# Kernel optimization log

Measured on AMD Instinct MI355X. Metric: run time of the kernel, lower is better.

Reference implementation:

```python
import jax, jax.numpy as jnp
import numpy as np

B, L, D, N, K = 4, 4096, 1024, 64, 3
EPS = 1e-6

def setup_inputs() -> dict:
    key = jax.random.key(0)
    ks = jax.random.split(key, 24)
    f32 = jnp.float32
    inp = {
        'T': jax.random.normal(ks[0], (B, L, D), f32),
        'norm_scale': jnp.ones((D,), f32),
        'in_w': jax.random.normal(ks[1], (2 * D, D), f32) * (1.0 / np.sqrt(D)),
        'in_b': jnp.zeros((2 * D,), f32),
        'dw_w': jax.random.normal(ks[2], (D, 1, K), f32) * (1.0 / np.sqrt(K)),
        'dw_b': jnp.zeros((D,), f32),
        'pw_w': jax.random.normal(ks[3], (D, D), f32) * (1.0 / np.sqrt(D)),
        'pw_b': jnp.zeros((D,), f32),
        'f_win': jax.random.normal(ks[4], (N, D), f32) * (1.0 / np.sqrt(D)),
        'f_wout': jax.random.normal(ks[5], (D, N), f32) * (1.0 / np.sqrt(N)),
        'f_logA': jax.random.normal(ks[6], (N,), f32) * 0.02,
        'f_B': jax.random.normal(ks[7], (N,), f32) * 0.02,
        'f_C': jax.random.normal(ks[8], (N,), f32) * 0.02,
        'f_logdt': jnp.array(0.0, f32),
        'b_win': jax.random.normal(ks[9], (N, D), f32) * (1.0 / np.sqrt(D)),
        'b_wout': jax.random.normal(ks[10], (D, N), f32) * (1.0 / np.sqrt(N)),
        'b_logA': jax.random.normal(ks[11], (N,), f32) * 0.02,
        'b_B': jax.random.normal(ks[12], (N,), f32) * 0.02,
        'b_C': jax.random.normal(ks[13], (N,), f32) * 0.02,
        'b_logdt': jnp.array(0.0, f32),
        'out_w': jax.random.normal(ks[14], (D, D), f32) * (1.0 / np.sqrt(D)),
        'out_b': jnp.zeros((D,), f32),
    }
    return inp

def _ssm(x, win, wout, logA, Bp, Cp, logdt):
    # ZOH discretization of diagonal SSM
    dt = jnp.exp(logdt)
    A = -jnp.exp(logA)
    Abar = jnp.exp(A * dt)
    denom = jnp.where(jnp.abs(A) < EPS, jnp.ones_like(A), A)
    frac = jnp.where(jnp.abs(A) < EPS, dt, (Abar - 1.0) / denom)
    Bbar = frac * Bp
    u = jnp.einsum('bld,nd->bln', x, win)  # (B,L,N)
    h0 = jnp.zeros((x.shape[0], win.shape[0]), x.dtype)
    def step(h, ut):
        h = h * Abar + ut * Bbar
        return h, h * Cp
    _, ys = jax.lax.scan(step, h0, jnp.swapaxes(u, 0, 1))  # (L,B,N)
    y = jnp.swapaxes(ys, 0, 1)
    return jnp.einsum('bln,dn->bld', y, wout)

def reference(T, norm_scale, in_w, in_b, dw_w, dw_b, pw_w, pw_b,
              f_win, f_wout, f_logA, f_B, f_C, f_logdt,
              b_win, b_wout, b_logA, b_B, b_C, b_logdt,
              out_w, out_b):
    # RMSNorm
    rms = jnp.sqrt(jnp.mean(T * T, axis=-1, keepdims=True) + EPS)
    Tn = T / rms * norm_scale
    # in_linear -> chunk
    xz = Tn @ in_w.T + in_b
    x, z = jnp.split(xz, 2, axis=-1)
    gate = jax.nn.sigmoid(z)
    # depthwise-separable conv1d (NCH layout)
    xc = jnp.swapaxes(x, 1, 2)  # (B,D,L)
    xc = jax.lax.conv_general_dilated(
        xc, dw_w, window_strides=(1,), padding=[(K // 2, K // 2)],
        dimension_numbers=('NCH', 'OIH', 'NCH'), feature_group_count=D)
    xc = xc + dw_b[None, :, None]
    xc = jnp.einsum('bdl,ed->bel', xc, pw_w) + pw_b[None, :, None]
    x_conv = jnp.swapaxes(xc, 1, 2)  # (B,L,D)
    # bidirectional SSM
    y_f = _ssm(x_conv, f_win, f_wout, f_logA, f_B, f_C, f_logdt)
    y_b = _ssm(jnp.flip(x_conv, axis=1), b_win, b_wout, b_logA, b_B, b_C, b_logdt)
    y_b = jnp.flip(y_b, axis=1)
    y = (y_f + y_b) * gate
    y = y @ out_w.T + out_b
    return T + y
```

## Files before the change

kernel.cpp:

```cpp
#include <hip/hip_runtime.h>
#include <cstdint>


#define L_SEQ 4096
#define D_DIM 1024
#define B_SZ 4
#define M_TOK (B_SZ * L_SEQ)
#define CHUNKS 64
#define CLEN (L_SEQ / CHUNKS)

typedef short bf16x8 __attribute__((ext_vector_type(8)));
typedef float floatx4 __attribute__((ext_vector_type(4)));

__device__ inline unsigned short f2bf(float f) {
  union { float f; unsigned int u; } v; v.f = f;
  unsigned int r = v.u + 0x7FFFu + ((v.u >> 16) & 1u);
  return (unsigned short)(r >> 16);
}
__device__ inline float bf2f(unsigned short h) {
  union { unsigned int u; float f; } v; v.u = ((unsigned int)h) << 16;
  return v.f;
}

__device__ inline void load_lds16(const unsigned short* g, unsigned short* l) {
  __builtin_amdgcn_global_load_lds(
      (const __attribute__((address_space(1))) unsigned int*)g,
      (__attribute__((address_space(3))) unsigned int*)l, 16, 0, 0);
}

__global__ __launch_bounds__(256) void rmsnorm_kernel(
    const float* __restrict__ T, const float* __restrict__ scale,
    unsigned short* __restrict__ Tn) {
  int tok = blockIdx.x;
  int t = threadIdx.x;
  const float4* row = (const float4*)(T + (size_t)tok * D_DIM);
  float4 v = row[t];
  float ss = v.x*v.x + v.y*v.y + v.z*v.z + v.w*v.w;
  #pragma unroll
  for (int off = 32; off > 0; off >>= 1) ss += __shfl_down(ss, off);
  __shared__ float part[4];
  if ((t & 63) == 0) part[t >> 6] = ss;
  __syncthreads();
  float total = part[0] + part[1] + part[2] + part[3];
  float rinv = rsqrtf(total * (1.0f / D_DIM) + 1e-6f);
  const float4* sc4 = (const float4*)scale;
  float4 s = sc4[t];
  ushort4 o;
  o.x = f2bf(v.x * rinv * s.x); o.y = f2bf(v.y * rinv * s.y);
  o.z = f2bf(v.z * rinv * s.z); o.w = f2bf(v.w * rinv * s.w);
  ((ushort4*)(Tn + (size_t)tok * D_DIM))[t] = o;
}

__global__ __launch_bounds__(256) void f2bf_vec_kernel(
    const float* __restrict__ in, unsigned short* __restrict__ out, int n4) {
  int i = blockIdx.x * 256 + threadIdx.x;
  if (i < n4) {
    float4 v = ((const float4*)in)[i];
    ushort4 o; o.x = f2bf(v.x); o.y = f2bf(v.y); o.z = f2bf(v.z); o.w = f2bf(v.w);
    ((ushort4*)out)[i] = o;
  }
}

__global__ void prepack_kernel(
    const float* __restrict__ f_win, const float* __restrict__ b_win,
    const float* __restrict__ f_wout, const float* __restrict__ b_wout,
    unsigned short* __restrict__ Wu, unsigned short* __restrict__ Wy) {
  int i = blockIdx.x * blockDim.x + threadIdx.x;
  if (i < 128 * D_DIM) {
    int n = i >> 10, k = i & (D_DIM - 1);
    Wu[i] = f2bf((n < 64) ? f_win[n * D_DIM + k] : b_win[(n - 64) * D_DIM + k]);
    int d = i >> 7, kk = i & 127;
    Wy[i] = f2bf((kk < 64) ? f_wout[d * 64 + kk] : b_wout[d * 64 + (kk - 64)]);
  }
}

template<int MODE, typename OUT_T>
__global__ __launch_bounds__(256) void gemm_mfma_kernel(
    const unsigned short* __restrict__ A, const unsigned short* __restrict__ Bw,
    const float* __restrict__ bias, OUT_T* __restrict__ out,
    int M, int N, int Kt,
    const void* __restrict__ aux0, unsigned short* __restrict__ aux1) {
  __shared__ unsigned short As[2 * 128 * 32];
  __shared__ unsigned short Bs[2 * 128 * 32];
  int tid = threadIdx.x;
  int wave = tid >> 6, lane = tid & 63;
  int quad = lane >> 4, lrow = lane & 15;
  int bm = blockIdx.y * 128, bn = blockIdx.x * 128;
  int wm = (wave & 1) * 64, wn = (wave >> 1) * 64;

  int r0 = tid >> 2;
  int c8 = (tid & 3) * 8;
  const unsigned short* Ag0 = A  + (size_t)(bm + r0) * Kt + c8;
  const unsigned short* Ag1 = A  + (size_t)(bm + 64 + r0) * Kt + c8;
  const unsigned short* Bg0 = Bw + (size_t)(bn + r0) * Kt + c8;
  const unsigned short* Bg1 = Bw + (size_t)(bn + 64 + r0) * Kt + c8;
  unsigned short* Al0 = As + (size_t)wave * 512;
  unsigned short* Al1 = As + 2048 + (size_t)wave * 512;
  unsigned short* Bl0 = Bs + (size_t)wave * 512;
  unsigned short* Bl1 = Bs + 2048 + (size_t)wave * 512;

  floatx4 acc[4][4] = {};
  for (int k0 = 0; k0 < Kt; k0 += 64) {
    load_lds16(Ag0 + k0, Al0);
    load_lds16(Ag1 + k0, Al1);
    load_lds16(Bg0 + k0, Bl0);
    load_lds16(Bg1 + k0, Bl1);
    load_lds16(Ag0 + k0 + 32, Al0 + 4096);
    load_lds16(Ag1 + k0 + 32, Al1 + 4096);
    load_lds16(Bg0 + k0 + 32, Bl0 + 4096);
    load_lds16(Bg1 + k0 + 32, Bl1 + 4096);
    __syncthreads();
    #pragma unroll
    for (int ks = 0; ks < 2; ++ks) {
      const unsigned short* Ab = As + ks * 4096;
      const unsigned short* Bb = Bs + ks * 4096;
      bf16x8 af[4], bfr[4];
      #pragma unroll
      for (int mi = 0; mi < 4; ++mi)
        af[mi] = *(const bf16x8*)(Ab + (wm + mi * 16 + lrow) * 32 + quad * 8);
      #pragma unroll
      for (int ni = 0; ni < 4; ++ni)
        bfr[ni] = *(const bf16x8*)(Bb + (wn + ni * 16 + lrow) * 32 + quad * 8);
      #pragma unroll
      for (int mi = 0; mi < 4; ++mi)
        #pragma unroll
        for (int ni = 0; ni < 4; ++ni)
          acc[mi][ni] = __builtin_amdgcn_mfma_f32_16x16x32_bf16(
              af[mi], bfr[ni], acc[mi][ni], 0, 0, 0);
    }
    __syncthreads();
  }

  #pragma unroll
  for (int mi = 0; mi < 4; ++mi) {
    #pragma unroll
    for (int ni = 0; ni < 4; ++ni) {
      #pragma unroll
      for (int r = 0; r < 4; ++r) {
        int m = bm + wm + mi * 16 + quad * 4 + r;
        int n = bn + wn + ni * 16 + lrow;
        float v = acc[mi][ni][r];
        if (MODE == 0) {
          if (bias) v += bias[n];
          if (sizeof(OUT_T) == 2) out[(size_t)m * N + n] = (OUT_T)f2bf(v);
          else                    out[(size_t)m * N + n] = (OUT_T)v;
        } else if (MODE == 1) {
          if (bias) v += bias[n];
          if (n < D_DIM) ((unsigned short*)out)[(size_t)m * D_DIM + n] = f2bf(v);
          else aux1[(size_t)m * D_DIM + (n - D_DIM)] = f2bf(1.0f / (1.0f + expf(-v)));
        } else if (MODE == 2) {
          v *= bf2f(((const unsigned short*)aux0)[(size_t)m * N + n]);
          ((unsigned short*)out)[(size_t)m * N + n] = f2bf(v);
        } else {
          if (bias) v += bias[n];
          v += ((const float*)aux0)[(size_t)m * N + n];
          ((float*)out)[(size_t)m * N + n] = v;
        }
      }
    }
  }
}

__global__ __launch_bounds__(256) void dwconv_kernel(
    const unsigned short* __restrict__ x, const float* __restrict__ w,
    const float* __restrict__ b, unsigned short* __restrict__ out) {
  size_t i8 = (size_t)blockIdx.x * 256 + threadIdx.x;
  int d8 = (int)(i8 & (D_DIM / 8 - 1));
  size_t tok = i8 >> 7;
  int l = (int)(tok & (L_SEQ - 1));
  int d0 = d8 * 8;
  size_t base = tok * D_DIM + d0;
  bf16x8 cur = *(const bf16x8*)(x + base);
  float acc[8];
  #pragma unroll
  for (int j = 0; j < 8; ++j) {
    int d = d0 + j;
    acc[j] = b[d] + w[d * 3 + 1] * bf2f((unsigned short)cur[j]);
  }
  if (l > 0) {
    bf16x8 prv = *(const bf16x8*)(x + base - D_DIM);
    #pragma unroll
    for (int j = 0; j < 8; ++j) acc[j] += w[(d0 + j) * 3 + 0] * bf2f((unsigned short)prv[j]);
  }
  if (l < L_SEQ - 1) {
    bf16x8 nxt = *(const bf16x8*)(x + base + D_DIM);
    #pragma unroll
    for (int j = 0; j < 8; ++j) acc[j] += w[(d0 + j) * 3 + 2] * bf2f((unsigned short)nxt[j]);
  }
  bf16x8 o;
  #pragma unroll
  for (int j = 0; j < 8; ++j) o[j] = (short)f2bf(acc[j]);
  *(bf16x8*)(out + base) = o;
}

__device__ inline void ssm_params(
    int col,
    const float* f_logA, const float* f_B, const float* f_C, const float* f_logdt,
    const float* b_logA, const float* b_B, const float* b_C, const float* b_logdt,
    float& Abar, float& Bbar, float& Cc, float& Aa, float& dt) {
  int dir = col >> 6, n = col & 63;
  const float* logA  = dir ? b_logA  : f_logA;
  const float* Bp    = dir ? b_B     : f_B;
  const float* Cp    = dir ? b_C     : f_C;
  const float* logdt = dir ? b_logdt : f_logdt;
  dt = expf(logdt[0]);
  Aa = -expf(logA[n]);
  Abar = expf(Aa * dt);
  float frac = (fabsf(Aa) < 1e-6f) ? dt : (Abar - 1.0f) / Aa;
  Bbar = frac * Bp[n];
  Cc = Cp[n];
}

__global__ __launch_bounds__(128) void scan_s1_kernel(
    const float* __restrict__ u, float* __restrict__ states,
    const float* __restrict__ f_logA, const float* __restrict__ f_B,
    const float* __restrict__ f_C, const float* __restrict__ f_logdt,
    const float* __restrict__ b_logA, const float* __restrict__ b_B,
    const float* __restrict__ b_C, const float* __restrict__ b_logdt) {
  int col = threadIdx.x;
  int chunk = blockIdx.x, b = blockIdx.y;
  float Abar, Bbar, Cc, Aa, dt;
  ssm_params(col, f_logA, f_B, f_C, f_logdt, b_logA, b_B, b_C, b_logdt,
             Abar, Bbar, Cc, Aa, dt);
  size_t base = ((size_t)b * L_SEQ + (size_t)chunk * CLEN) * 128 + col;
  float h = 0.0f;
  if (col < 64) {
    for (int i0 = 0; i0 < CLEN; i0 += 8) {
      float uv[8];
      #pragma unroll
      for (int j = 0; j < 8; ++j) uv[j] = u[base + (size_t)(i0 + j) * 128];
      #pragma unroll
      for (int j = 0; j < 8; ++j) h = h * Abar + uv[j] * Bbar;
    }
  } else {
    for (int i0 = CLEN - 1; i0 >= 0; i0 -= 8) {
      float uv[8];
      #pragma unroll
      for (int j = 0; j < 8; ++j) uv[j] = u[base + (size_t)(i0 - j) * 128];
      #pragma unroll
      for (int j = 0; j < 8; ++j) h = h * Abar + uv[j] * Bbar;
    }
  }
  states[((size_t)b * CHUNKS + chunk) * 128 + col] = h;
}

__global__ __launch_bounds__(512) void scan_s2_kernel(
    const float* __restrict__ states, float* __restrict__ carries,
    const float* __restrict__ f_logA, const float* __restrict__ f_B,
    const float* __restrict__ f_C, const float* __restrict__ f_logdt,
    const float* __restrict__ b_logA, const float* __restrict__ b_B,
    const float* __restrict__ b_C, const float* __restrict__ b_logdt) {
  int tid = threadIdx.x;
  int b = tid >> 7, col = tid & 127;
  float Abar, Bbar, Cc, Aa, dt;
  ssm_params(col, f_logA, f_B, f_C, f_logdt, b_logA, b_B, b_C, b_logdt,
             Abar, Bbar, Cc, Aa, dt);
  float Ac = expf(Aa * dt * (float)CLEN);
  size_t sb = (size_t)b * CHUNKS * 128 + col;
  float cur = 0.0f;
  if (col < 64) {
    for (int c = 0; c < CHUNKS; ++c) {
      carries[sb + (size_t)c * 128] = cur;
      cur = cur * Ac + states[sb + (size_t)c * 128];
    }
  } else {
    for (int c = CHUNKS - 1; c >= 0; --c) {
      carries[sb + (size_t)c * 128] = cur;
      cur = cur * Ac + states[sb + (size_t)c * 128];
    }
  }
}

__global__ __launch_bounds__(128) void scan_s3_kernel(
    const float* __restrict__ u, const float* __restrict__ carries,
    unsigned short* __restrict__ y,
    const float* __restrict__ f_logA, const float* __restrict__ f_B,
    const float* __restrict__ f_C, const float* __restrict__ f_logdt,
    const float* __restrict__ b_logA, const float* __restrict__ b_B,
    const float* __restrict__ b_C, const float* __restrict__ b_logdt) {
  int col = threadIdx.x;
  int chunk = blockIdx.x, b = blockIdx.y;
  float Abar, Bbar, Cc, Aa, dt;
  ssm_params(col, f_logA, f_B, f_C, f_logdt, b_logA, b_B, b_C, b_logdt,
             Abar, Bbar, Cc, Aa, dt);
  size_t base = ((size_t)b * L_SEQ + (size_t)chunk * CLEN) * 128 + col;
  float h = carries[((size_t)b * CHUNKS + chunk) * 128 + col];
  if (col < 64) {
    for (int i0 = 0; i0 < CLEN; i0 += 8) {
      float uv[8];
      #pragma unroll
      for (int j = 0; j < 8; ++j) uv[j] = u[base + (size_t)(i0 + j) * 128];
      #pragma unroll
      for (int j = 0; j < 8; ++j) {
        h = h * Abar + uv[j] * Bbar;
        y[base + (size_t)(i0 + j) * 128] = f2bf(h * Cc);
      }
    }
  } else {
    for (int i0 = CLEN - 1; i0 >= 0; i0 -= 8) {
      float uv[8];
      #pragma unroll
      for (int j = 0; j < 8; ++j) uv[j] = u[base + (size_t)(i0 - j) * 128];
      #pragma unroll
      for (int j = 0; j < 8; ++j) {
        h = h * Abar + uv[j] * Bbar;
        y[base + (size_t)(i0 - j) * 128] = f2bf(h * Cc);
      }
    }
  }
}

extern "C" void kernel_launch(void* const* d_in, const int* in_sizes, int n_in,
                              void* d_out, int out_size, void* d_ws, size_t ws_size,
                              hipStream_t stream) {
  const float* T         = (const float*)d_in[0];
  const float* norm_scale= (const float*)d_in[1];
  const float* in_w      = (const float*)d_in[2];
  const float* in_b      = (const float*)d_in[3];
  const float* dw_w      = (const float*)d_in[4];
  const float* dw_b      = (const float*)d_in[5];
  const float* pw_w      = (const float*)d_in[6];
  const float* pw_b      = (const float*)d_in[7];
  const float* f_win     = (const float*)d_in[8];
  const float* f_wout    = (const float*)d_in[9];
  const float* f_logA    = (const float*)d_in[10];
  const float* f_B       = (const float*)d_in[11];
  const float* f_C       = (const float*)d_in[12];
  const float* f_logdt   = (const float*)d_in[13];
  const float* b_win     = (const float*)d_in[14];
  const float* b_wout    = (const float*)d_in[15];
  const float* b_logA    = (const float*)d_in[16];
  const float* b_B       = (const float*)d_in[17];
  const float* b_C       = (const float*)d_in[18];
  const float* b_logdt   = (const float*)d_in[19];
  const float* out_w     = (const float*)d_in[20];
  const float* out_b     = (const float*)d_in[21];
  float* out = (float*)d_out;

  char* ws = (char*)d_ws;
  const size_t MD = (size_t)M_TOK * D_DIM;
  unsigned short* gate  = (unsigned short*)ws;              ws += MD * 2;
  unsigned short* bufA  = (unsigned short*)ws;              ws += MD * 2;
  unsigned short* bufB  = (unsigned short*)ws;              ws += MD * 2;
  float*          u     = (float*)ws;                       ws += (size_t)M_TOK * 128 * 4;
  unsigned short* ybuf  = (unsigned short*)ws;              ws += (size_t)M_TOK * 128 * 2;
  unsigned short* w_in  = (unsigned short*)ws;              ws += (size_t)2 * D_DIM * D_DIM * 2;
  unsigned short* w_pw  = (unsigned short*)ws;              ws += (size_t)D_DIM * D_DIM * 2;
  unsigned short* w_out = (unsigned short*)ws;              ws += (size_t)D_DIM * D_DIM * 2;
  unsigned short* Wu    = (unsigned short*)ws;              ws += (size_t)128 * D_DIM * 2;
  unsigned short* Wy    = (unsigned short*)ws;              ws += (size_t)128 * D_DIM * 2;
  float*          states= (float*)ws;                       ws += (size_t)B_SZ * CHUNKS * 128 * 4;
  float*          carries=(float*)ws;

  f2bf_vec_kernel<<<(2 * D_DIM * D_DIM / 4 + 255) / 256, 256, 0, stream>>>(in_w, w_in, 2 * D_DIM * D_DIM / 4);
  f2bf_vec_kernel<<<(D_DIM * D_DIM / 4 + 255) / 256, 256, 0, stream>>>(pw_w, w_pw, D_DIM * D_DIM / 4);
  f2bf_vec_kernel<<<(D_DIM * D_DIM / 4 + 255) / 256, 256, 0, stream>>>(out_w, w_out, D_DIM * D_DIM / 4);
  prepack_kernel<<<(128 * D_DIM) / 256, 256, 0, stream>>>(f_win, b_win, f_wout, b_wout, Wu, Wy);
  rmsnorm_kernel<<<M_TOK, 256, 0, stream>>>(T, norm_scale, bufA);
  {
    dim3 g((2 * D_DIM) / 128, M_TOK / 128);
    gemm_mfma_kernel<1, unsigned short><<<g, 256, 0, stream>>>(
        bufA, w_in, in_b, bufB, M_TOK, 2 * D_DIM, D_DIM, nullptr, gate);
  }
  dwconv_kernel<<<(MD / 8) / 256, 256, 0, stream>>>(bufB, dw_w, dw_b, bufA);
  {
    dim3 g(D_DIM / 128, M_TOK / 128);
    gemm_mfma_kernel<0, unsigned short><<<g, 256, 0, stream>>>(
        bufA, w_pw, pw_b, bufB, M_TOK, D_DIM, D_DIM, nullptr, nullptr);
  }
  {
    dim3 g(1, M_TOK / 128);
    gemm_mfma_kernel<0, float><<<g, 256, 0, stream>>>(
        bufB, Wu, nullptr, u, M_TOK, 128, D_DIM, nullptr, nullptr);
  }
  {
    dim3 g1(CHUNKS, B_SZ);
    scan_s1_kernel<<<g1, 128, 0, stream>>>(u, states, f_logA, f_B, f_C, f_logdt,
                                           b_logA, b_B, b_C, b_logdt);
    scan_s2_kernel<<<1, 512, 0, stream>>>(states, carries, f_logA, f_B, f_C, f_logdt,
                                          b_logA, b_B, b_C, b_logdt);
    scan_s3_kernel<<<g1, 128, 0, stream>>>(u, carries, ybuf, f_logA, f_B, f_C, f_logdt,
                                           b_logA, b_B, b_C, b_logdt);
  }
  {
    dim3 g(D_DIM / 128, M_TOK / 128);
    gemm_mfma_kernel<2, unsigned short><<<g, 256, 0, stream>>>(
        ybuf, Wy, nullptr, bufA, M_TOK, D_DIM, 128, gate, nullptr);
  }
  {
    dim3 g(D_DIM / 128, M_TOK / 128);
    gemm_mfma_kernel<3, float><<<g, 256, 0, stream>>>(
        bufA, w_out, out_b, out, M_TOK, D_DIM, D_DIM, T, nullptr);
  }
}
```

Baseline: 634.7 us.

## Double-buffer GEMM LDS tiles to overlap global loads with MFMA compute

The GEMM main loop now splits LDS into two buffers of a 32-wide K slice each. It prefetches the next slice into the other buffer while the MFMAs run on the current one, so each iteration needs one barrier instead of two. It also raises wave priority around the MFMA block with s_setprio. The loop runs twice as many iterations with half the work each, so per-iteration overhead grows. How much overlap is gained depends on how load_lds16 is implemented (direct-to-LDS versus through registers).

```diff
diff --git a/kernel.cpp b/kernel.cpp
--- a/kernel.cpp
+++ b/kernel.cpp
@@ -80,8 +80,8 @@
     const float* __restrict__ bias, OUT_T* __restrict__ out,
     int M, int N, int Kt,
     const void* __restrict__ aux0, unsigned short* __restrict__ aux1) {
-  __shared__ unsigned short As[2 * 128 * 32];
-  __shared__ unsigned short Bs[2 * 128 * 32];
+  __shared__ unsigned short As[2][128 * 32];
+  __shared__ unsigned short Bs[2][128 * 32];
   int tid = threadIdx.x;
   int wave = tid >> 6, lane = tid & 63;
   int quad = lane >> 4, lrow = lane & 15;
@@ -94,26 +94,30 @@
   const unsigned short* Ag1 = A  + (size_t)(bm + 64 + r0) * Kt + c8;
   const unsigned short* Bg0 = Bw + (size_t)(bn + r0) * Kt + c8;
   const unsigned short* Bg1 = Bw + (size_t)(bn + 64 + r0) * Kt + c8;
-  unsigned short* Al0 = As + (size_t)wave * 512;
-  unsigned short* Al1 = As + 2048 + (size_t)wave * 512;
-  unsigned short* Bl0 = Bs + (size_t)wave * 512;
-  unsigned short* Bl1 = Bs + 2048 + (size_t)wave * 512;
+  int woff = wave * 512;
 
   floatx4 acc[4][4] = {};
-  for (int k0 = 0; k0 < Kt; k0 += 64) {
-    load_lds16(Ag0 + k0, Al0);
-    load_lds16(Ag1 + k0, Al1);
-    load_lds16(Bg0 + k0, Bl0);
-    load_lds16(Bg1 + k0, Bl1);
-    load_lds16(Ag0 + k0 + 32, Al0 + 4096);
-    load_lds16(Ag1 + k0 + 32, Al1 + 4096);
-    load_lds16(Bg0 + k0 + 32, Bl0 + 4096);
-    load_lds16(Bg1 + k0 + 32, Bl1 + 4096);
-    __syncthreads();
-    #pragma unroll
-    for (int ks = 0; ks < 2; ++ks) {
-      const unsigned short* Ab = As + ks * 4096;
-      const unsigned short* Bb = Bs + ks * 4096;
+  int nt = Kt >> 5;
+
+  load_lds16(Ag0, &As[0][0] + woff);
+  load_lds16(Ag1, &As[0][0] + 2048 + woff);
+  load_lds16(Bg0, &Bs[0][0] + woff);
+  load_lds16(Bg1, &Bs[0][0] + 2048 + woff);
+  __syncthreads();
+
+  int cur = 0;
+  for (int t = 0; t < nt; ++t) {
+    if (t + 1 < nt) {
+      int k0 = (t + 1) << 5;
+      int nb = cur ^ 1;
+      load_lds16(Ag0 + k0, &As[nb][0] + woff);
+      load_lds16(Ag1 + k0, &As[nb][0] + 2048 + woff);
+      load_lds16(Bg0 + k0, &Bs[nb][0] + woff);
+      load_lds16(Bg1 + k0, &Bs[nb][0] + 2048 + woff);
+    }
+    {
+      const unsigned short* Ab = &As[cur][0];
+      const unsigned short* Bb = &Bs[cur][0];
       bf16x8 af[4], bfr[4];
       #pragma unroll
       for (int mi = 0; mi < 4; ++mi)
@@ -121,14 +125,19 @@
       #pragma unroll
       for (int ni = 0; ni < 4; ++ni)
         bfr[ni] = *(const bf16x8*)(Bb + (wn + ni * 16 + lrow) * 32 + quad * 8);
+      __builtin_amdgcn_s_setprio(1);
       #pragma unroll
       for (int mi = 0; mi < 4; ++mi)
         #pragma unroll
         for (int ni = 0; ni < 4; ++ni)
           acc[mi][ni] = __builtin_amdgcn_mfma_f32_16x16x32_bf16(
               af[mi], bfr[ni], acc[mi][ni], 0, 0, 0);
-    }
-    __syncthreads();
+      __builtin_amdgcn_s_setprio(0);
+    }
+    if (t + 1 < nt) {
+      __syncthreads();
+      cur ^= 1;
+    }
   }
 
   #pragma unroll
```

After: 622.0 us. 2.0% less time.
